# Kernel optimization log

Measured on AMD Instinct MI355X. Metric: run time of the kernel, lower is better.

The kernel has to match this reference:

```python
import jax, jax.numpy as jnp
import numpy as np

V, H, B, S, T = 512, 1024, 128, 256, 128


def setup_inputs() -> dict:
    key = jax.random.key(0)
    ks = jax.random.split(key, 16)
    s = 1.0 / np.sqrt(H)
    f32 = jnp.float32
    return {
        "encoder_outputs": jax.random.normal(ks[0], (B, S, H), f32),
        "encoder_hidden": jax.random.normal(ks[1], (1, B, H), f32),
        "encoder_cell": jax.random.normal(ks[2], (1, B, H), f32),
        "target_tensor": jax.random.randint(ks[3], (B, T), 0, V),
        "max_length": T,
        "emb": (jax.random.normal(ks[4], (V, H), f32) * s),
        "Wa_w": jax.random.normal(ks[5], (H, H), f32) * s,
        "Wa_b": jnp.zeros((H,), f32),
        "Ua_w": jax.random.normal(ks[6], (H, H), f32) * s,
        "Ua_b": jnp.zeros((H,), f32),
        "Va_w": jax.random.normal(ks[7], (1, H), f32) * s,
        "Va_b": jnp.zeros((1,), f32),
        "W_ih": jax.random.normal(ks[8], (4 * H, 2 * H), f32) * s,
        "W_hh": jax.random.normal(ks[9], (4 * H, H), f32) * s,
        "b_ih": jnp.zeros((4 * H,), f32),
        "b_hh": jnp.zeros((4 * H,), f32),
        "out_w": jax.random.normal(ks[10], (V, H), f32) * s,
        "out_b": jnp.zeros((V,), f32),
    }


def reference(encoder_outputs, encoder_hidden, encoder_cell, target_tensor, max_length,
              emb, Wa_w, Wa_b, Ua_w, Ua_b, Va_w, Va_b,
              W_ih, W_hh, b_ih, b_hh, out_w, out_b):
    # Teacher forcing: decoder input at step i is SOS (=0) then target[:, i-1].
    bsz = encoder_outputs.shape[0]
    sos = jnp.zeros((bsz, 1), dtype=target_tensor.dtype)
    tokens = jnp.concatenate([sos, target_tensor[:, : max_length - 1]], axis=1)  # [B, T]
    xs = emb[tokens].transpose(1, 0, 2)  # [T, B, H] (dropout = identity, eval mode)

    # Ua(keys) is loop-invariant (original recomputes it each step; same math).
    keys_proj = jnp.einsum('bsh,kh->bsk', encoder_outputs, Ua_w) + Ua_b  # [B, S, H]

    def step(carry, emb_t):
        h, c = carry  # [B, H] each
        q = h @ Wa_w.T + Wa_b  # Bahdanau query projection [B, H]
        e = jnp.tanh(q[:, None, :] + keys_proj) @ Va_w[0] + Va_b[0]  # [B, S]
        w = jax.nn.softmax(e, axis=-1)
        ctx = jnp.einsum('bs,bsh->bh', w, encoder_outputs)
        x = jnp.concatenate([emb_t, ctx], axis=-1)  # [B, 2H]
        gates = x @ W_ih.T + b_ih + h @ W_hh.T + b_hh  # [B, 4H], torch order i,f,g,o
        i, f, g, o = jnp.split(gates, 4, axis=-1)
        c_new = jax.nn.sigmoid(f) * c + jax.nn.sigmoid(i) * jnp.tanh(g)
        h_new = jax.nn.sigmoid(o) * jnp.tanh(c_new)
        logits = h_new @ out_w.T + out_b  # [B, V]
        return (h_new, c_new), (logits, w)

    init = (encoder_hidden[0], encoder_cell[0])
    (h_fin, c_fin), (logits, attn) = jax.lax.scan(step, init, xs)
    log_probs = jax.nn.log_softmax(logits.transpose(1, 0, 2), axis=-1)  # [B, T, V]
    return log_probs, h_fin[None], attn.transpose(1, 0, 2)  # hidden [1,B,H], attn [B,T,S]
```

## Files before the change

### kernel.cpp

```cpp
#include <hip/hip_runtime.h>

#define B_ 128
#define S_ 256
#define H_ 1024
#define V_ 512
#define T_ 128
#define G4 4096

typedef __attribute__((ext_vector_type(8))) short bf16x8;
typedef __attribute__((ext_vector_type(4))) float f32x4;
typedef __attribute__((ext_vector_type(2))) float f32x2;

__device__ __forceinline__ float bf2f(unsigned short x) {
    unsigned int u = ((unsigned int)x) << 16;
    return __builtin_bit_cast(float, u);
}
__device__ __forceinline__ unsigned short f2b(float f) {
    unsigned int u = __builtin_bit_cast(unsigned int, f);
    u = u + 0x7fffu + ((u >> 16) & 1u);
    return (unsigned short)(u >> 16);
}
__device__ __forceinline__ float ftanh(float x) {
    float e = __expf(2.f * x);
    return 1.f - 2.f * __builtin_amdgcn_rcpf(e + 1.f);
}
__device__ __forceinline__ float fsigm(float x) {
    return __builtin_amdgcn_rcpf(1.f + __expf(-x));
}
__device__ __forceinline__ void gll16(const void* g, void* l) {
    __builtin_amdgcn_global_load_lds(
        (const __attribute__((address_space(1))) unsigned int*)g,
        (__attribute__((address_space(3))) unsigned int*)l, 16, 0, 0);
}

__device__ __forceinline__ unsigned char sw_e4m3(float f) {
    unsigned int ub = __builtin_bit_cast(unsigned int, f);
    unsigned char s = (unsigned char)((ub >> 24) & 0x80);
    float a = fabsf(f);
    if (!(a < 464.f)) return (unsigned char)(s | 0x7E);
    if (a < 0.0009765625f) return s;
    if (a < 0.015625f) {
        int m = (int)(a * 512.f + 0.5f);
        if (m >= 8) return (unsigned char)(s | 0x08);
        return (unsigned char)(s | m);
    }
    unsigned int u = __builtin_bit_cast(unsigned int, a);
    u += 0x7FFFF + ((u >> 20) & 1);
    int e = (int)(u >> 23) - 127;
    if (e > 8) return (unsigned char)(s | 0x7E);
    unsigned int man = (u >> 20) & 7;
    return (unsigned char)(s | ((unsigned int)(e + 7) << 3) | man);
}
__device__ __forceinline__ float sw_f_e4m3(unsigned int byte) {
    unsigned int s = (byte & 0x80u) << 24;
    unsigned int em = byte & 0x7Fu;
    float v;
    if (em >= 8u) v = __builtin_bit_cast(float, (em + 960u) << 20);
    else v = (float)em * 0.001953125f;
    return __builtin_bit_cast(float, __builtin_bit_cast(unsigned int, v) | s);
}
__device__ __forceinline__ unsigned char enc1(float a) {
#if __has_builtin(__builtin_amdgcn_cvt_pk_fp8_f32)
    unsigned int w = __builtin_amdgcn_cvt_pk_fp8_f32(a, a, 0u, false);
    return (unsigned char)(w & 0xff);
#else
    return sw_e4m3(a);
#endif
}
__device__ __forceinline__ unsigned int enc4(float a, float b, float c, float d) {
#if __has_builtin(__builtin_amdgcn_cvt_pk_fp8_f32)
    unsigned int w = 0;
    w = __builtin_amdgcn_cvt_pk_fp8_f32(a, b, w, false);
    w = __builtin_amdgcn_cvt_pk_fp8_f32(c, d, w, true);
    return w;
#else
    return (unsigned int)sw_e4m3(a) | ((unsigned int)sw_e4m3(b) << 8) |
           ((unsigned int)sw_e4m3(c) << 16) | ((unsigned int)sw_e4m3(d) << 24);
#endif
}
__device__ __forceinline__ void dec4(unsigned int w, float* o) {
#if __has_builtin(__builtin_amdgcn_cvt_pk_f32_fp8)
    f32x2 lo = __builtin_amdgcn_cvt_pk_f32_fp8(w, false);
    f32x2 hi = __builtin_amdgcn_cvt_pk_f32_fp8(w, true);
    o[0] = lo.x; o[1] = lo.y; o[2] = hi.x; o[3] = hi.y;
#else
    o[0] = sw_f_e4m3(w & 0xff); o[1] = sw_f_e4m3((w >> 8) & 0xff);
    o[2] = sw_f_e4m3((w >> 16) & 0xff); o[3] = sw_f_e4m3(w >> 24);
#endif
}

__global__ void f32_to_bf16_x4(const float4* __restrict__ in, ushort4* __restrict__ out, int n4) {
    int i = blockIdx.x * 256 + threadIdx.x;
    if (i < n4) {
        float4 v = in[i];
        ushort4 o;
        o.x = f2b(v.x); o.y = f2b(v.y); o.z = f2b(v.z); o.w = f2b(v.w);
        out[i] = o;
    }
}

__global__ void f32_to_fp8_x4(const float4* __restrict__ in, unsigned int* __restrict__ out, int n4) {
    int i = blockIdx.x * 256 + threadIdx.x;
    if (i < n4) {
        float4 v = in[i];
        out[i] = enc4(v.x, v.y, v.z, v.w);
    }
}

__global__ void cvt_gather(const float* __restrict__ src, int src_ld, int coff,
                           unsigned short* __restrict__ dst, int perm) {
    int i = blockIdx.x * 256 + threadIdx.x;
    int r = i >> 8;
    int c = (i & 255) * 4;
    int sr = perm ? (((r & 3) << 10) + (r >> 2)) : r;
    float4 v = *reinterpret_cast<const float4*>(src + (size_t)sr * src_ld + coff + c);
    ushort4 o;
    o.x = f2b(v.x); o.y = f2b(v.y); o.z = f2b(v.z); o.w = f2b(v.w);
    *reinterpret_cast<ushort4*>(dst + (size_t)r * 1024 + c) = o;
}

__global__ void build_toks(const int* __restrict__ target, int* __restrict__ toks) {
    int idx = blockIdx.x * 256 + threadIdx.x;
    if (idx < T_ * B_) {
        int t = idx / B_, b = idx % B_;
        toks[idx] = (t == 0) ? 0 : target[b * T_ + t - 1];
    }
}

__global__ void build_bsum(const float* __restrict__ b_ih, const float* __restrict__ b_hh,
                           float* __restrict__ bsum) {
    int j = blockIdx.x * 256 + threadIdx.x;
    if (j < G4) {
        int pj = ((j & 3) << 10) + (j >> 2);
        bsum[j] = b_ih[pj] + b_hh[pj];
    }
}

template<int MODE>
__global__ __launch_bounds__(256) void gemm_mf(
    const unsigned short* __restrict__ A,
    const unsigned short* __restrict__ Bw,
    int K, int ldb, int ldc,
    float* __restrict__ C, unsigned char* __restrict__ C8,
    const float* __restrict__ bias)
{
    __shared__ unsigned short As[2 * 8192];
    __shared__ unsigned short Bs[2 * 8192];
    const int tid = threadIdx.x;
    const int lane = tid & 63;
    const int wv = tid >> 6;
    const int m0 = blockIdx.x * 64;
    const int n0 = blockIdx.y * 64;

    const unsigned short* ga[4];
    const unsigned short* gb[4];
    #pragma unroll
    for (int j = 0; j < 4; ++j) {
        int ci = tid + 256 * j;
        int row = ci >> 4;
        int src = (ci & 15) ^ (row & 7);
        ga[j] = A + (size_t)(m0 + row) * K + src * 8;
        gb[j] = Bw + (size_t)(n0 + row) * ldb + src * 8;
    }

    f32x4 acc[2][2] = {};
    const int r0 = (wv >> 1) * 32;
    const int cq0 = (wv & 1) * 32;
    const int fr = lane & 15;
    const int kg = lane >> 4;

    auto stage = [&](int k0, int p) {
        #pragma unroll
        for (int j = 0; j < 4; ++j) {
            gll16(ga[j] + k0, As + p * 8192 + j * 2048 + wv * 512);
            gll16(gb[j] + k0, Bs + p * 8192 + j * 2048 + wv * 512);
        }
    };

    stage(0, 0);
    stage(128, 1);
    int p = 0;
    for (int k0 = 0; k0 < K; k0 += 128) {
        if (k0 + 128 < K) {
            asm volatile("s_waitcnt vmcnt(8)" ::: "memory");
        } else {
            asm volatile("s_waitcnt vmcnt(0)" ::: "memory");
        }
        __builtin_amdgcn_sched_barrier(0);
        __builtin_amdgcn_s_barrier();
        __builtin_amdgcn_sched_barrier(0);
        const unsigned short* Ab = As + p * 8192;
        const unsigned short* Bb = Bs + p * 8192;
        bf16x8 af[2][4], bfr[2][4];
        #pragma unroll
        for (int f = 0; f < 2; ++f)
            #pragma unroll
            for (int kh = 0; kh < 4; ++kh) {
                int ra = r0 + f * 16 + fr;
                af[f][kh] = *(const bf16x8*)&Ab[ra * 128 + (((kh * 4 + kg) ^ (ra & 7)) << 3)];
                int rb = cq0 + f * 16 + fr;
                bfr[f][kh] = *(const bf16x8*)&Bb[rb * 128 + (((kh * 4 + kg) ^ (rb & 7)) << 3)];
            }
        asm volatile("s_waitcnt lgkmcnt(0)" ::: "memory");
        __builtin_amdgcn_sched_barrier(0);
        __builtin_amdgcn_s_barrier();
        __builtin_amdgcn_sched_barrier(0);
        if (k0 + 256 < K) stage(k0 + 256, p);
        __builtin_amdgcn_s_setprio(1);
        #pragma unroll
        for (int f = 0; f < 2; ++f)
            #pragma unroll
            for (int g = 0; g < 2; ++g)
                #pragma unroll
                for (int kh = 0; kh < 4; ++kh)
                    acc[f][g] = __builtin_amdgcn_mfma_f32_16x16x32_bf16(
                        af[f][kh], bfr[g][kh], acc[f][g], 0, 0, 0);
        __builtin_amdgcn_s_setprio(0);
        p ^= 1;
    }

    const int erow = (lane >> 4) * 4;
    const int ecol = lane & 15;
    #pragma unroll
    for (int f = 0; f < 2; ++f) {
        #pragma unroll
        for (int g = 0; g < 2; ++g) {
            #pragma unroll
            for (int r = 0; r < 4; ++r) {
                int row = m0 + r0 + f * 16 + erow + r;
                int col = n0 + cq0 + g * 16 + ecol;
                float v = acc[f][g][r] + bias[col];
                if (MODE == 0) C[(size_t)row * ldc + col] = v;
                else C8[(size_t)row * ldc + col] = enc1(v);
            }
        }
    }
}

template<int MODE>
__global__ __launch_bounds__(256) void gemm_n32(
    const unsigned short* __restrict__ A,
    const unsigned short* __restrict__ Bw,
    int K, int ldb, int ldc,
    float* __restrict__ C, unsigned short* __restrict__ Cb,
    const float* __restrict__ bias,
    const float* __restrict__ Pemb,
    const int* __restrict__ toks,
    float* __restrict__ Cq,
    float* __restrict__ Lg,
    const float* __restrict__ bias2,
    int flag)
{
    __shared__ unsigned short As[3 * 8192];
    __shared__ unsigned short Bs[3 * 4096];
    const int tid = threadIdx.x;
    const int lane = tid & 63;
    const int wv = tid >> 6;
    const int m0 = blockIdx.x * 64;
    const int n0 = blockIdx.y * 32;

    const unsigned short* ga[4];
    const unsigned short* gb[2];
    #pragma unroll
    for (int j = 0; j < 4; ++j) {
        int ci = tid + 256 * j;
        int row = ci >> 4;
        int src = (ci & 15) ^ (row & 7);
        ga[j] = A + (size_t)(m0 + row) * K + src * 8;
    }
    #pragma unroll
    for (int j = 0; j < 2; ++j) {
        int ci = tid + 256 * j;
        int row = ci >> 4;
        int src = (ci & 15) ^ (row & 7);
        gb[j] = Bw + (size_t)(n0 + row) * ldb + src * 8;
    }

    f32x4 acc[2] = {};
    const int r0 = (wv >> 1) * 32;
    const int c0 = (wv & 1) * 16;
    const int fr = lane & 15;
    const int kg = lane >> 4;

    auto stage = [&](int k0, int p) {
        #pragma unroll
        for (int j = 0; j < 4; ++j)
            gll16(ga[j] + k0, As + p * 8192 + j * 2048 + wv * 512);
        #pragma unroll
        for (int j = 0; j < 2; ++j)
            gll16(gb[j] + k0, Bs + p * 4096 + j * 2048 + wv * 512);
    };

    stage(0, 0);
    stage(128, 1);
    stage(256, 2);
    int p = 0;
    for (int k0 = 0; k0 < K; k0 += 128) {
        if (k0 + 256 < K) {
            asm volatile("s_waitcnt vmcnt(12)" ::: "memory");
        } else if (k0 + 128 < K) {
            asm volatile("s_waitcnt vmcnt(6)" ::: "memory");
        } else {
            asm volatile("s_waitcnt vmcnt(0)" ::: "memory");
        }
        __builtin_amdgcn_sched_barrier(0);
        __builtin_amdgcn_s_barrier();
        __builtin_amdgcn_sched_barrier(0);
        const unsigned short* Ab = As + p * 8192;
        const unsigned short* Bb = Bs + p * 4096;
        bf16x8 af[2][4], bfr[4];
        #pragma unroll
        for (int kh = 0; kh < 4; ++kh) {
            #pragma unroll
            for (int f = 0; f < 2; ++f) {
                int ra = r0 + f * 16 + fr;
                af[f][kh] = *(const bf16x8*)&Ab[ra * 128 + (((kh * 4 + kg) ^ (ra & 7)) << 3)];
            }
            int rb = c0 + fr;
            bfr[kh] = *(const bf16x8*)&Bb[rb * 128 + (((kh * 4 + kg) ^ (rb & 7)) << 3)];
        }
        asm volatile("s_waitcnt lgkmcnt(0)" ::: "memory");
        __builtin_amdgcn_sched_barrier(0);
        __builtin_amdgcn_s_barrier();
        __builtin_amdgcn_sched_barrier(0);
        if (k0 + 384 < K) stage(k0 + 384, p);
        __builtin_amdgcn_s_setprio(1);
        #pragma unroll
        for (int f = 0; f < 2; ++f)
            #pragma unroll
            for (int kh = 0; kh < 4; ++kh)
                acc[f] = __builtin_amdgcn_mfma_f32_16x16x32_bf16(
                    af[f][kh], bfr[kh], acc[f], 0, 0, 0);
        __builtin_amdgcn_s_setprio(0);
        p = (p == 2) ? 0 : p + 1;
    }

    const int erow = (lane >> 4) * 4;
    const int ecol = lane & 15;

    if constexpr (MODE == 4) {
        __shared__ float Lt[64 * 32];
        __syncthreads();
        #pragma unroll
        for (int f = 0; f < 2; ++f)
            #pragma unroll
            for (int r = 0; r < 4; ++r)
                Lt[(r0 + f * 16 + erow + r) * 32 + c0 + ecol] = acc[f][r];
        __syncthreads();
        #pragma unroll
        for (int i = 0; i < 2; ++i) {
            int pi = tid + 256 * i;
            int r = pi >> 3, u = pi & 7;
            int b = m0 + r;
            int hh = (n0 >> 2) + u;
            f32x4 gv = *reinterpret_cast<const f32x4*>(&Lt[r * 32 + u * 4]);
            const float* gp = C + (size_t)b * G4 + n0 + u * 4;
            float iv = gv[0] + gp[0];
            float fv = gv[1] + gp[1];
            float gg = gv[2] + gp[2];
            float ov = gv[3] + gp[3];
            int ci = b * H_ + hh;
            float cn = fsigm(fv) * Cq[ci] + fsigm(iv) * ftanh(gg);
            float hn = fsigm(ov) * ftanh(cn);
            Cq[ci] = cn;
            Cb[ci] = f2b(hn);
            if (flag) Lg[ci] = hn;
        }
    } else {
        #pragma unroll
        for (int f = 0; f < 2; ++f) {
            #pragma unroll
            for (int r = 0; r < 4; ++r) {
                int row = m0 + r0 + f * 16 + erow + r;
                int col = n0 + c0 + ecol;
                float v = acc[f][r];
                if (MODE == 0) {
                    C[(size_t)row * ldc + col] = v + bias[col];
                } else {
                    if (col < H_) {
                        Cq[(size_t)row * H_ + col] = v + bias[col];
                    } else if (col < 5120) {
                        int cg = col - H_;
                        C[(size_t)row * G4 + cg] = v + Pemb[(size_t)toks[row] * G4 + cg];
                    } else {
                        int cl = col - 5120;
                        Lg[(size_t)row * V_ + cl] = v + bias2[cl];
                    }
                }
            }
        }
    }
}

__global__ __launch_bounds__(256) void attn_e(
    const unsigned int* __restrict__ kp8,
    const float* __restrict__ q,
    const float* __restrict__ Va,
    const unsigned int* __restrict__ encb8,
    float* __restrict__ es_g,
    unsigned short* __restrict__ pctx,
    const float* __restrict__ lg,
    float* __restrict__ lp,
    int t)
{
    const int b = blockIdx.x;
    const int sh = blockIdx.y;
    const int tid = threadIdx.x;
    const int lane = tid & 63;
    const int wv = tid >> 6;
    __shared__ float qs[H_];
    __shared__ float vas[H_];
    __shared__ float pe[16];
    __shared__ float redm[4], reds[4];

    *reinterpret_cast<float4*>(&qs[tid * 4]) =
        *reinterpret_cast<const float4*>(&q[(size_t)b * H_ + tid * 4]);
    *reinterpret_cast<float4*>(&vas[tid * 4]) =
        *reinterpret_cast<const float4*>(&Va[tid * 4]);

    const bool doL = (t > 0) && (sh == 0);
    float a0 = doL ? lg[(size_t)b * V_ + tid] : -3.4e38f;
    float a1 = doL ? lg[(size_t)b * V_ + 256 + tid] : -3.4e38f;
    float mx = fmaxf(a0, a1);
    #pragma unroll
    for (int off = 32; off; off >>= 1) mx = fmaxf(mx, __shfl_xor(mx, off));
    if (lane == 0) redm[wv] = mx;
    __syncthreads();
    mx = fmaxf(fmaxf(redm[0], redm[1]), fmaxf(redm[2], redm[3]));
    float sm = doL ? (__expf(a0 - mx) + __expf(a1 - mx)) : 0.f;
    #pragma unroll
    for (int off = 32; off; off >>= 1) sm += __shfl_xor(sm, off);
    if (lane == 0) reds[wv] = sm;
    __syncthreads();
    if (doL) {
        sm = reds[0] + reds[1] + reds[2] + reds[3];
        float lse = mx + __logf(sm);
        size_t off = ((size_t)b * T_ + (t - 1)) * V_;
        lp[off + tid] = a0 - lse;
        lp[off + tid + 256] = a1 - lse;
    }

    #pragma unroll
    for (int si = 0; si < 4; ++si) {
        int s_loc = wv * 4 + si;
        const uint4* kr = reinterpret_cast<const uint4*>(
            kp8 + (size_t)(b * S_ + sh * 16 + s_loc) * 256);
        uint4 u = kr[lane];
        const int h0 = lane * 16;
        float d[4];
        float acc = 0.f;
        dec4(u.x, d);
        acc += vas[h0 + 0] * ftanh(qs[h0 + 0] + d[0]);
        acc += vas[h0 + 1] * ftanh(qs[h0 + 1] + d[1]);
        acc += vas[h0 + 2] * ftanh(qs[h0 + 2] + d[2]);
        acc += vas[h0 + 3] * ftanh(qs[h0 + 3] + d[3]);
        dec4(u.y, d);
        acc += vas[h0 + 4] * ftanh(qs[h0 + 4] + d[0]);
        acc += vas[h0 + 5] * ftanh(qs[h0 + 5] + d[1]);
        acc += vas[h0 + 6] * ftanh(qs[h0 + 6] + d[2]);
        acc += vas[h0 + 7] * ftanh(qs[h0 + 7] + d[3]);
        dec4(u.z, d);
        acc += vas[h0 + 8] * ftanh(qs[h0 + 8] + d[0]);
        acc += vas[h0 + 9] * ftanh(qs[h0 + 9] + d[1]);
        acc += vas[h0 + 10] * ftanh(qs[h0 + 10] + d[2]);
        acc += vas[h0 + 11] * ftanh(qs[h0 + 11] + d[3]);
        dec4(u.w, d);
        acc += vas[h0 + 12] * ftanh(qs[h0 + 12] + d[0]);
        acc += vas[h0 + 13] * ftanh(qs[h0 + 13] + d[1]);
        acc += vas[h0 + 14] * ftanh(qs[h0 + 14] + d[2]);
        acc += vas[h0 + 15] * ftanh(qs[h0 + 15] + d[3]);
        #pragma unroll
        for (int off = 32; off; off >>= 1) acc += __shfl_down(acc, off);
        if (lane == 0) {
            pe[s_loc] = __expf(acc);
            es_g[(size_t)b * S_ + sh * 16 + s_loc] = acc;
        }
    }
    __syncthreads();

    const int c0 = tid * 4;
    float ax = 0.f, ay = 0.f, az = 0.f, aw = 0.f;
    #pragma unroll
    for (int sl = 0; sl < 16; ++sl) {
        unsigned int u = encb8[(size_t)(b * S_ + sh * 16 + sl) * 256 + tid];
        float d[4];
        dec4(u, d);
        float w = pe[sl];
        ax += w * d[0];
        ay += w * d[1];
        az += w * d[2];
        aw += w * d[3];
    }
    ushort4 o4;
    o4.x = f2b(ax); o4.y = f2b(ay); o4.z = f2b(az); o4.w = f2b(aw);
    *reinterpret_cast<ushort4*>(&pctx[((size_t)b * 16 + sh) * H_ + c0]) = o4;
}

__global__ __launch_bounds__(256) void attn_comb(
    const float* __restrict__ es_g,
    const unsigned short* __restrict__ pctx,
    unsigned short* __restrict__ ctxb,
    float* __restrict__ attnOut,
    int t)
{
    const int b = blockIdx.x;
    const int hh = blockIdx.y;
    const int tid = threadIdx.x;
    const int lane = tid & 63;
    const int wv = tid >> 6;
    __shared__ float reds[4];

    float ex = __expf(es_g[(size_t)b * S_ + tid]);
    float sm = ex;
    #pragma unroll
    for (int off = 32; off; off >>= 1) sm += __shfl_xor(sm, off);
    if (lane == 0) reds[wv] = sm;
    __syncthreads();
    sm = reds[0] + reds[1] + reds[2] + reds[3];
    float rZ = __builtin_amdgcn_rcpf(sm);
    if (hh == 0) attnOut[((size_t)(b * T_ + t)) * S_ + tid] = ex * rZ;

    const int c0 = hh * 512 + tid * 2;
    float a0 = 0.f, a1 = 0.f;
    #pragma unroll
    for (int blk = 0; blk < 16; ++blk) {
        ushort2 pv = *reinterpret_cast<const ushort2*>(
            &pctx[((size_t)b * 16 + blk) * H_ + c0]);
        a0 += bf2f(pv.x); a1 += bf2f(pv.y);
    }
    ushort2 o; o.x = f2b(a0 * rZ); o.y = f2b(a1 * rZ);
    *reinterpret_cast<ushort2*>(&ctxb[(size_t)b * H_ + c0]) = o;
}

__global__ __launch_bounds__(256) void lsm_kernel(
    const float* __restrict__ lg, float* __restrict__ lp, int t)
{
    int b = blockIdx.x, tid = threadIdx.x;
    int lane = tid & 63, wv = tid >> 6;
    __shared__ float red[4];
    float a0 = lg[(size_t)b * V_ + tid];
    float a1 = lg[(size_t)b * V_ + 256 + tid];
    float mx = fmaxf(a0, a1);
    #pragma unroll
    for (int off = 32; off; off >>= 1) mx = fmaxf(mx, __shfl_xor(mx, off));
    if (lane == 0) red[wv] = mx;
    __syncthreads();
    mx = fmaxf(fmaxf(red[0], red[1]), fmaxf(red[2], red[3]));
    float sm = __expf(a0 - mx) + __expf(a1 - mx);
    #pragma unroll
    for (int off = 32; off; off >>= 1) sm += __shfl_xor(sm, off);
    __syncthreads();
    if (lane == 0) red[wv] = sm;
    __syncthreads();
    sm = red[0] + red[1] + red[2] + red[3];
    float lse = mx + __logf(sm);
    size_t off = ((size_t)b * T_ + t) * V_;
    lp[off + tid] = a0 - lse;
    lp[off + tid + 256] = a1 - lse;
}

extern "C" void kernel_launch(void* const* d_in, const int* in_sizes, int n_in,
                              void* d_out, int out_size, void* d_ws, size_t ws_size,
                              hipStream_t stream) {
    const float* enc   = (const float*)d_in[0];
    const float* h0    = (const float*)d_in[1];
    const float* c0    = (const float*)d_in[2];
    const int*   targ  = (const int*)d_in[3];
    const float* emb   = (const float*)d_in[5];
    const float* Wa_w  = (const float*)d_in[6];
    const float* Wa_b  = (const float*)d_in[7];
    const float* Ua_w  = (const float*)d_in[8];
    const float* Ua_b  = (const float*)d_in[9];
    const float* Va_w  = (const float*)d_in[10];
    const float* W_ih  = (const float*)d_in[12];
    const float* W_hh  = (const float*)d_in[13];
    const float* b_ih  = (const float*)d_in[14];
    const float* b_hh  = (const float*)d_in[15];
    const float* out_w = (const float*)d_in[16];
    const float* out_b = (const float*)d_in[17];

    float* out  = (float*)d_out;
    float* lp   = out;
    float* hid  = out + (size_t)B_ * T_ * V_;
    float* attn = hid + (size_t)B_ * H_;

    char* w = (char*)d_ws;
    auto alloc = [&](size_t bytes) {
        char* p = w;
        w += (bytes + 255) & ~(size_t)255;
        return p;
    };
    const size_t NKP = (size_t)B_ * S_ * H_;
    unsigned int* kp8      = (unsigned int*)alloc(NKP);
    unsigned int* encb8    = (unsigned int*)alloc(NKP);
    unsigned short* encb   = (unsigned short*)alloc(NKP * 2);
    unsigned short* Wcat_b = (unsigned short*)alloc((size_t)5632 * H_ * 2);
    unsigned short* Wih1_b = (unsigned short*)alloc((size_t)G4 * H_ * 2);
    unsigned short* Wih2_b = (unsigned short*)alloc((size_t)G4 * H_ * 2);
    unsigned short* Uaw_b  = (unsigned short*)alloc((size_t)H_ * H_ * 2);
    unsigned short* emb_b  = (unsigned short*)alloc((size_t)V_ * H_ * 2);
    unsigned short* hb     = (unsigned short*)alloc((size_t)B_ * H_ * 2);
    unsigned short* ctxb   = (unsigned short*)alloc((size_t)B_ * H_ * 2);
    float* Pemb  = (float*)alloc((size_t)V_ * G4 * 4);
    float* bsumP = (float*)alloc((size_t)G4 * 4);
    int*   toks  = (int*)alloc((size_t)T_ * B_ * 4);
    float* cbuf  = (float*)alloc((size_t)B_ * H_ * 4);
    float* qbuf  = (float*)alloc((size_t)B_ * H_ * 4);
    float* gates = (float*)alloc((size_t)B_ * G4 * 4);
    float* lgbuf = (float*)alloc((size_t)B_ * V_ * 4);
    float* es_g  = (float*)alloc((size_t)B_ * S_ * 4);
    unsigned short* pctx = (unsigned short*)alloc((size_t)B_ * 16 * H_ * 2);
    if ((size_t)(w - (char*)d_ws) > ws_size) return;

    auto cvt = [&](const float* src, unsigned short* dst, size_t n) {
        int n4 = (int)(n / 4);
        f32_to_bf16_x4<<<(n4 + 255) / 256, 256, 0, stream>>>((const float4*)src, (ushort4*)dst, n4);
    };

    cvt(enc, encb, NKP);
    f32_to_fp8_x4<<<(int)(NKP / 4 + 255) / 256, 256, 0, stream>>>(
        (const float4*)enc, encb8, (int)(NKP / 4));
    cvt(Ua_w, Uaw_b, (size_t)H_ * H_);
    cvt(emb, emb_b, (size_t)V_ * H_);
    cvt(h0, hb, (size_t)B_ * H_);
    cvt_gather<<<1024, 256, 0, stream>>>(Wa_w, H_, 0, Wcat_b, 0);
    cvt_gather<<<4096, 256, 0, stream>>>(W_hh, H_, 0, Wcat_b + (size_t)1024 * H_, 1);
    cvt_gather<<<512, 256, 0, stream>>>(out_w, H_, 0, Wcat_b + (size_t)5120 * H_, 0);
    cvt_gather<<<4096, 256, 0, stream>>>(W_ih, 2 * H_, 0, Wih1_b, 1);
    cvt_gather<<<4096, 256, 0, stream>>>(W_ih, 2 * H_, H_, Wih2_b, 1);
    build_toks<<<(T_ * B_ + 255) / 256, 256, 0, stream>>>(targ, toks);
    build_bsum<<<(G4 + 255) / 256, 256, 0, stream>>>(b_ih, b_hh, bsumP);
    hipMemcpyAsync(cbuf, c0, (size_t)B_ * H_ * 4, hipMemcpyDeviceToDevice, stream);

    gemm_mf<1><<<dim3((B_ * S_) / 64, H_ / 64), 256, 0, stream>>>(
        encb, Uaw_b, H_, H_, H_, nullptr, (unsigned char*)kp8, Ua_b);
    gemm_mf<0><<<dim3(V_ / 64, G4 / 64), 256, 0, stream>>>(
        emb_b, Wih1_b, H_, H_, G4, Pemb, nullptr, bsumP);

    for (int t = 0; t < T_; ++t) {
        gemm_n32<2><<<dim3(2, 176), 256, 0, stream>>>(
            hb, Wcat_b, H_, H_, 0, gates, nullptr, Wa_b,
            Pemb, toks + t * B_, qbuf, lgbuf, out_b, 0);
        attn_e<<<dim3(B_, 16), 256, 0, stream>>>(
            kp8, qbuf, Va_w, encb8, es_g, pctx, lgbuf, lp, t);
        attn_comb<<<dim3(B_, 2), 256, 0, stream>>>(es_g, pctx, ctxb, attn, t);
        gemm_n32<4><<<dim3(2, 128), 256, 0, stream>>>(
            ctxb, Wih2_b, H_, H_, 0, gates, hb, nullptr,
            nullptr, nullptr, cbuf, hid, nullptr, t == T_ - 1);
    }
    gemm_n32<0><<<dim3(2, 16), 256, 0, stream>>>(
        hb, Wcat_b + (size_t)5120 * H_, H_, H_, V_, lgbuf, nullptr, out_b,
        nullptr, nullptr, nullptr, nullptr, nullptr, 0);
    lsm_kernel<<<B_, 256, 0, stream>>>(lgbuf, lp, T_ - 1);
}
```

Before: 5.655 ms.

## Hoist output projection and log-softmax out of the recurrent loop into one batched GEMM

Each step's hidden state is now stored in a per-step buffer that reuses the bf16 encoder-copy workspace. The per-step output-projection columns are dropped from the fused recurrent GEMM, and the log-softmax work is dropped from the attention kernel. After the loop, a single large GEMM computes logits for all T*B rows, followed by one log-softmax kernel. This shortens the serial per-step critical path and uses the GPU far better for the vocab projection. The cost is extra workspace traffic and reusing the encb region after it has been consumed.

```diff
diff --git a/kernel.cpp b/kernel.cpp
--- a/kernel.cpp
+++ b/kernel.cpp
@@ -248,7 +248,6 @@
     const int* __restrict__ toks,
     float* __restrict__ Cq,
     float* __restrict__ Lg,
-    const float* __restrict__ bias2,
     int flag)
 {
     __shared__ unsigned short As[3 * 8192];
@@ -379,12 +378,9 @@
                 } else {
                     if (col < H_) {
                         Cq[(size_t)row * H_ + col] = v + bias[col];
-                    } else if (col < 5120) {
+                    } else {
                         int cg = col - H_;
                         C[(size_t)row * G4 + cg] = v + Pemb[(size_t)toks[row] * G4 + cg];
-                    } else {
-                        int cl = col - 5120;
-                        Lg[(size_t)row * V_ + cl] = v + bias2[cl];
                     }
                 }
             }
@@ -398,10 +394,7 @@
     const float* __restrict__ Va,
     const unsigned int* __restrict__ encb8,
     float* __restrict__ es_g,
-    unsigned short* __restrict__ pctx,
-    const float* __restrict__ lg,
-    float* __restrict__ lp,
-    int t)
+    unsigned short* __restrict__ pctx)
 {
     const int b = blockIdx.x;
     const int sh = blockIdx.y;
@@ -411,34 +404,12 @@
     __shared__ float qs[H_];
     __shared__ float vas[H_];
     __shared__ float pe[16];
-    __shared__ float redm[4], reds[4];
 
     *reinterpret_cast<float4*>(&qs[tid * 4]) =
         *reinterpret_cast<const float4*>(&q[(size_t)b * H_ + tid * 4]);
     *reinterpret_cast<float4*>(&vas[tid * 4]) =
         *reinterpret_cast<const float4*>(&Va[tid * 4]);
-
-    const bool doL = (t > 0) && (sh == 0);
-    float a0 = doL ? lg[(size_t)b * V_ + tid] : -3.4e38f;
-    float a1 = doL ? lg[(size_t)b * V_ + 256 + tid] : -3.4e38f;
-    float mx = fmaxf(a0, a1);
-    #pragma unroll
-    for (int off = 32; off; off >>= 1) mx = fmaxf(mx, __shfl_xor(mx, off));
-    if (lane == 0) redm[wv] = mx;
     __syncthreads();
-    mx = fmaxf(fmaxf(redm[0], redm[1]), fmaxf(redm[2], redm[3]));
-    float sm = doL ? (__expf(a0 - mx) + __expf(a1 - mx)) : 0.f;
-    #pragma unroll
-    for (int off = 32; off; off >>= 1) sm += __shfl_xor(sm, off);
-    if (lane == 0) reds[wv] = sm;
-    __syncthreads();
-    if (doL) {
-        sm = reds[0] + reds[1] + reds[2] + reds[3];
-        float lse = mx + __logf(sm);
-        size_t off = ((size_t)b * T_ + (t - 1)) * V_;
-        lp[off + tid] = a0 - lse;
-        lp[off + tid + 256] = a1 - lse;
-    }
 
     #pragma unroll
     for (int si = 0; si < 4; ++si) {
@@ -532,14 +503,17 @@
     *reinterpret_cast<ushort2*>(&ctxb[(size_t)b * H_ + c0]) = o;
 }
 
-__global__ __launch_bounds__(256) void lsm_kernel(
-    const float* __restrict__ lg, float* __restrict__ lp, int t)
+__global__ __launch_bounds__(256) void lsm_all(
+    const float* __restrict__ lgall,
+    float* __restrict__ lp)
 {
-    int b = blockIdx.x, tid = threadIdx.x;
+    int r = blockIdx.x;
+    int t = r >> 7, b = r & (B_ - 1);
+    int tid = threadIdx.x;
     int lane = tid & 63, wv = tid >> 6;
     __shared__ float red[4];
-    float a0 = lg[(size_t)b * V_ + tid];
-    float a1 = lg[(size_t)b * V_ + 256 + tid];
+    float a0 = lgall[(size_t)r * V_ + tid];
+    float a1 = lgall[(size_t)r * V_ + 256 + tid];
     float mx = fmaxf(a0, a1);
     #pragma unroll
     for (int off = 32; off; off >>= 1) mx = fmaxf(mx, __shfl_xor(mx, off));
@@ -593,13 +567,17 @@
     const size_t NKP = (size_t)B_ * S_ * H_;
     unsigned int* kp8      = (unsigned int*)alloc(NKP);
     unsigned int* encb8    = (unsigned int*)alloc(NKP);
-    unsigned short* encb   = (unsigned short*)alloc(NKP * 2);
-    unsigned short* Wcat_b = (unsigned short*)alloc((size_t)5632 * H_ * 2);
+    char* uni = alloc(NKP * 2);
+    unsigned short* encb = (unsigned short*)uni;
+    unsigned short* hall = (unsigned short*)uni;
+    float* lgall = (float*)(uni + (size_t)T_ * B_ * H_ * 2);
+    unsigned short* Wcat_b = (unsigned short*)alloc((size_t)5120 * H_ * 2);
     unsigned short* Wih1_b = (unsigned short*)alloc((size_t)G4 * H_ * 2);
     unsigned short* Wih2_b = (unsigned short*)alloc((size_t)G4 * H_ * 2);
     unsigned short* Uaw_b  = (unsigned short*)alloc((size_t)H_ * H_ * 2);
     unsigned short* emb_b  = (unsigned short*)alloc((size_t)V_ * H_ * 2);
-    unsigned short* hb     = (unsigned short*)alloc((size_t)B_ * H_ * 2);
+    unsigned short* owb_b  = (unsigned short*)alloc((size_t)V_ * H_ * 2);
+    unsigned short* hb0    = (unsigned short*)alloc((size_t)B_ * H_ * 2);
     unsigned short* ctxb   = (unsigned short*)alloc((size_t)B_ * H_ * 2);
     float* Pemb  = (float*)alloc((size_t)V_ * G4 * 4);
     float* bsumP = (float*)alloc((size_t)G4 * 4);
@@ -607,7 +585,6 @@
     float* cbuf  = (float*)alloc((size_t)B_ * H_ * 4);
     float* qbuf  = (float*)alloc((size_t)B_ * H_ * 4);
     float* gates = (float*)alloc((size_t)B_ * G4 * 4);
-    float* lgbuf = (float*)alloc((size_t)B_ * V_ * 4);
     float* es_g  = (float*)alloc((size_t)B_ * S_ * 4);
     unsigned short* pctx = (unsigned short*)alloc((size_t)B_ * 16 * H_ * 2);
     if ((size_t)(w - (char*)d_ws) > ws_size) return;
@@ -622,10 +599,10 @@
         (const float4*)enc, encb8, (int)(NKP / 4));
     cvt(Ua_w, Uaw_b, (size_t)H_ * H_);
     cvt(emb, emb_b, (size_t)V_ * H_);
-    cvt(h0, hb, (size_t)B_ * H_);
+    cvt(h0, hb0, (size_t)B_ * H_);
     cvt_gather<<<1024, 256, 0, stream>>>(Wa_w, H_, 0, Wcat_b, 0);
     cvt_gather<<<4096, 256, 0, stream>>>(W_hh, H_, 0, Wcat_b + (size_t)1024 * H_, 1);
-    cvt_gather<<<512, 256, 0, stream>>>(out_w, H_, 0, Wcat_b + (size_t)5120 * H_, 0);
+    cvt_gather<<<512, 256, 0, stream>>>(out_w, H_, 0, owb_b, 0);
     cvt_gather<<<4096, 256, 0, stream>>>(W_ih, 2 * H_, 0, Wih1_b, 1);
     cvt_gather<<<4096, 256, 0, stream>>>(W_ih, 2 * H_, H_, Wih2_b, 1);
     build_toks<<<(T_ * B_ + 255) / 256, 256, 0, stream>>>(targ, toks);
@@ -638,18 +615,19 @@
         emb_b, Wih1_b, H_, H_, G4, Pemb, nullptr, bsumP);
 
     for (int t = 0; t < T_; ++t) {
-        gemm_n32<2><<<dim3(2, 176), 256, 0, stream>>>(
-            hb, Wcat_b, H_, H_, 0, gates, nullptr, Wa_b,
-            Pemb, toks + t * B_, qbuf, lgbuf, out_b, 0);
-        attn_e<<<dim3(B_, 16), 256, 0, stream>>>(
-            kp8, qbuf, Va_w, encb8, es_g, pctx, lgbuf, lp, t);
+        const unsigned short* hprev = (t == 0) ? hb0 : hall + (size_t)(t - 1) * B_ * H_;
+        gemm_n32<2><<<dim3(2, 160), 256, 0, stream>>>(
+            hprev, Wcat_b, H_, H_, 0, gates, nullptr, Wa_b,
+            Pemb, toks + t * B_, qbuf, nullptr, 0);
+        attn_e<<<dim3(B_, 16), 256, 0, stream>>>(kp8, qbuf, Va_w, encb8, es_g, pctx);
         attn_comb<<<dim3(B_, 2), 256, 0, stream>>>(es_g, pctx, ctxb, attn, t);
         gemm_n32<4><<<dim3(2, 128), 256, 0, stream>>>(
-            ctxb, Wih2_b, H_, H_, 0, gates, hb, nullptr,
-            nullptr, nullptr, cbuf, hid, nullptr, t == T_ - 1);
-    }
-    gemm_n32<0><<<dim3(2, 16), 256, 0, stream>>>(
-        hb, Wcat_b + (size_t)5120 * H_, H_, H_, V_, lgbuf, nullptr, out_b,
-        nullptr, nullptr, nullptr, nullptr, nullptr, 0);
-    lsm_kernel<<<B_, 256, 0, stream>>>(lgbuf, lp, T_ - 1);
-}
+            ctxb, Wih2_b, H_, H_, 0, gates, hall + (size_t)t * B_ * H_, nullptr,
+            nullptr, nullptr, cbuf, hid, t == T_ - 1);
+    }
+
+    gemm_n32<0><<<dim3((T_ * B_) / 64, V_ / 32), 256, 0, stream>>>(
+        hall, owb_b, H_, H_, V_, lgall, nullptr, out_b,
+        nullptr, nullptr, nullptr, nullptr, 0);
+    lsm_all<<<T_ * B_, 256, 0, stream>>>(lgall, lp);
+}
```

New measurement: 5.612 ms. Within noise of the previous version (-0.7%).
